# Kernel optimization log

Hardware: AMD Instinct MI355X
Metric: run time of the kernel (lower is better)

## Reference

```python
import jax, jax.numpy as jnp
import numpy as np

N_NODES = 20000
N_EDGES = 320000
F_IN = 128
H = 4        # heads per layer
D = 128      # per-head hidden dim
NEG_SLOPE = 0.2


def setup_inputs() -> dict:
    key = jax.random.key(0)
    ks = jax.random.split(key, 14)
    s = 0.05
    inp = {
        "feats": jax.random.normal(ks[0], (N_NODES, F_IN), jnp.float32),
        "src": jax.random.randint(ks[1], (N_EDGES,), 0, N_NODES, jnp.int64),
        "dst": jax.random.randint(ks[2], (N_EDGES,), 0, N_NODES, jnp.int64),
        # layer 1: in F_IN -> H heads x D, flatten agg
        "W1": s * jax.random.normal(ks[3], (F_IN, H * D), jnp.float32),
        "al1": s * jax.random.normal(ks[4], (H, D), jnp.float32),
        "ar1": s * jax.random.normal(ks[5], (H, D), jnp.float32),
        "b1": jnp.zeros((H * D,), jnp.float32),
        # layer 2: in H*D -> H heads x D, mean agg
        "W2": s * jax.random.normal(ks[6], (H * D, H * D), jnp.float32),
        "al2": s * jax.random.normal(ks[7], (H, D), jnp.float32),
        "ar2": s * jax.random.normal(ks[8], (H, D), jnp.float32),
        "b2": jnp.zeros((H * D,), jnp.float32),
        # readout Linear(D, 1)
        "Wr": s * jax.random.normal(ks[9], (D, 1), jnp.float32),
        "br": jnp.zeros((1,), jnp.float32),
    }
    return inp


def _gat_conv(x, src, dst, W, al, ar, b, n_nodes):
    """dgl GATConv: per-head linear, edge softmax over incoming edges, scatter-sum."""
    h, d = al.shape
    z = (x @ W).reshape(n_nodes, h, d)                      # [N,H,D]
    el = jnp.einsum('nhd,hd->nh', z, al)                    # [N,H]
    er = jnp.einsum('nhd,hd->nh', z, ar)                    # [N,H]
    e = jax.nn.leaky_relu(el[src] + er[dst], NEG_SLOPE)     # [E,H]
    # numerically stable softmax grouped by destination node
    emax = jax.lax.stop_gradient(jax.ops.segment_max(e, dst, num_segments=n_nodes))
    a = jnp.exp(e - emax[dst])                              # [E,H]
    denom = jax.ops.segment_sum(a, dst, num_segments=n_nodes)
    alpha = a / jnp.maximum(denom[dst], 1e-9)               # [E,H]
    out = jax.ops.segment_sum(alpha[:, :, None] * z[src], dst, num_segments=n_nodes)
    return out + b.reshape(1, h, d)                         # [N,H,D]


def reference(feats, src, dst, W1, al1, ar1, b1, W2, al2, ar2, b2, Wr, br):
    n = feats.shape[0]
    h1 = _gat_conv(feats, src, dst, W1, al1, ar1, b1, n)    # [N,H,D]
    h1 = jax.nn.elu(h1.reshape(n, -1))                      # flatten heads -> [N,H*D]
    h2 = _gat_conv(h1, src, dst, W2, al2, ar2, b2, n)       # [N,H,D]
    h2 = h2.mean(axis=1)                                    # mean over heads -> [N,D]
    node_preds = h2 @ Wr + br                               # [N,1]
    return node_preds.sum(axis=0)                           # [1]
```

## Files before the change

kernel.cpp:

```cpp
#include <hip/hip_runtime.h>
#include <hip/hip_bf16.h>
#include <cstddef>

constexpr int NN = 20000;
constexpr int NE = 320000;
constexpr int NHEAD = 4;
constexpr int ND = 128;
constexpr int HD = 512;
constexpr int MPAD = 20096;
constexpr int SLOTS = 64;
constexpr float NEG_SLOPE = 0.2f;

using short8 = __attribute__((ext_vector_type(8))) short;
using f32x4 = __attribute__((ext_vector_type(4))) float;
using f32x2 = __attribute__((ext_vector_type(2))) float;

__device__ inline void gload16(const void* g, void* l) {
  __builtin_amdgcn_global_load_lds(
      (const __attribute__((address_space(1))) void*)g,
      (__attribute__((address_space(3))) void*)l, 16, 0, 0);
}

__device__ inline unsigned char f32_to_fp8(float v) {
  int pk = __builtin_amdgcn_cvt_pk_fp8_f32(v, v, 0, false);
  return (unsigned char)(pk & 0xff);
}

constexpr int S0 = NE;
constexpr int S1 = S0 + MPAD * 128;
constexpr int S2 = S1 + 512 * 128;
constexpr int S3 = S2 + 12 * 512;
constexpr int S4 = S3 + 256;
__global__ __launch_bounds__(256) void prep_kernel(
    const float* __restrict__ feats, const float* __restrict__ W1,
    const float* __restrict__ W2, const float* __restrict__ al2,
    const float* __restrict__ ar2, const float* __restrict__ Wr,
    const int* __restrict__ src, const int* __restrict__ dst,
    __hip_bfloat16* __restrict__ featsb, __hip_bfloat16* __restrict__ W1t,
    float* __restrict__ vcomb, float* __restrict__ partials,
    int* __restrict__ cnt, int* __restrict__ src_perm) {
  int t = blockIdx.x * 256 + threadIdx.x;
  if (t < S0) {
    int d = dst[t];
    int p = atomicAdd(&cnt[d], 1);
    if (p < SLOTS) src_perm[d * SLOTS + p] = src[t];
  } else if (t < S1) {
    int u = t - S0;
    featsb[u] = __float2bfloat16(u < NN * 128 ? feats[u] : 0.f);
  } else if (t < S2) {
    int u = t - S1;
    W1t[u] = __float2bfloat16(W1[(size_t)(u & 127) * 512 + (u >> 7)]);
  } else if (t < S3) {
    int u = t - S2;
    int v = u >> 9, k = u & 511;
    int h = (v < 4) ? v : (v < 8) ? v - 4 : v - 8;
    const float* vec = (v < 4) ? (al2 + h * 128)
                     : (v < 8) ? (ar2 + h * 128) : Wr;
    const float* wrow = W2 + (size_t)k * 512 + h * 128;
    float s = 0.f;
    for (int d = 0; d < 128; ++d) s += wrow[d] * vec[d];
    vcomb[u] = s;
  } else if (t < S4) {
    partials[t - S3] = 0.f;
  }
}

__global__ __launch_bounds__(256) void gemm1_kernel(
    const __hip_bfloat16* __restrict__ A,
    const __hip_bfloat16* __restrict__ Bt,
    unsigned char* __restrict__ C,
    const float* __restrict__ al, const float* __restrict__ ar,
    float* __restrict__ el, float* __restrict__ er) {
  constexpr int K = 128;
  __shared__ short As[128 * 32];
  __shared__ short Bs[128 * 32];
  __shared__ float elbuf[4][128];
  __shared__ float erbuf[4][128];
  int t = threadIdx.x;
  int lane = t & 63;
  int wave = t >> 6;
  int rowBase = blockIdx.x * 128;
  int head = blockIdx.y;
  int colBase = head * 128;
  int woffr = (wave & 1) * 64;
  int woffc = (wave >> 1) * 64;
  int mrow = lane & 15, quad = lane >> 4;

  f32x4 acc[4][4];
#pragma unroll
  for (int i = 0; i < 4; ++i)
#pragma unroll
    for (int j = 0; j < 4; ++j) acc[i][j] = (f32x4){0.f, 0.f, 0.f, 0.f};

  for (int k0 = 0; k0 < K; k0 += 32) {
#pragma unroll
    for (int p = 0; p < 2; ++p) {
      int f = p * 256 + wave * 64 + lane;
      int r = f >> 2, kc = f & 3;
      gload16(A + (size_t)(rowBase + r) * K + k0 + kc * 8,
              As + p * 2048 + wave * 512);
      gload16(Bt + (size_t)(colBase + r) * K + k0 + kc * 8,
              Bs + p * 2048 + wave * 512);
    }
    __syncthreads();
    short8 af[4], bfr[4];
#pragma unroll
    for (int i = 0; i < 4; ++i)
      af[i] = *(const short8*)&As[(woffr + i * 16 + mrow) * 32 + quad * 8];
#pragma unroll
    for (int j = 0; j < 4; ++j)
      bfr[j] = *(const short8*)&Bs[(woffc + j * 16 + mrow) * 32 + quad * 8];
#pragma unroll
    for (int i = 0; i < 4; ++i)
#pragma unroll
      for (int j = 0; j < 4; ++j)
        acc[i][j] = __builtin_amdgcn_mfma_f32_16x16x32_bf16(af[i], bfr[j], acc[i][j], 0, 0, 0);
    __syncthreads();
  }

#pragma unroll
  for (int i = 0; i < 4; ++i) {
#pragma unroll
    for (int j = 0; j < 4; ++j) {
      int col = colBase + woffc + j * 16 + mrow;
#pragma unroll
      for (int r = 0; r < 4; ++r) {
        int row = rowBase + woffr + i * 16 + quad * 4 + r;
        C[(size_t)row * HD + col] = f32_to_fp8(acc[i][j][r]);
      }
    }
  }

  float al_v[4], ar_v[4];
#pragma unroll
  for (int j = 0; j < 4; ++j) {
    int coll = woffc + j * 16 + mrow;
    al_v[j] = al[head * 128 + coll];
    ar_v[j] = ar[head * 128 + coll];
  }
#pragma unroll
  for (int i = 0; i < 4; ++i) {
#pragma unroll
    for (int r = 0; r < 4; ++r) {
      float pl = 0.f, pr = 0.f;
#pragma unroll
      for (int j = 0; j < 4; ++j) {
        float v = acc[i][j][r];
        pl += v * al_v[j];
        pr += v * ar_v[j];
      }
#pragma unroll
      for (int off = 1; off < 16; off <<= 1) {
        pl += __shfl_xor(pl, off);
        pr += __shfl_xor(pr, off);
      }
      if (mrow == 0) {
        int row128 = woffr + i * 16 + quad * 4 + r;
        elbuf[wave][row128] = pl;
        erbuf[wave][row128] = pr;
      }
    }
  }
  __syncthreads();
  if (t < 128) {
    int row = t;
    int w0 = (row < 64) ? 0 : 1;
    float ev = elbuf[w0][row] + elbuf[w0 + 2][row];
    float rv = erbuf[w0][row] + erbuf[w0 + 2][row];
    int gr = rowBase + row;
    if (gr < NN) {
      el[gr * 4 + head] = ev;
      er[gr * 4 + head] = rv;
    }
  }
}

__global__ __launch_bounds__(256) void aggregate_kernel(
    const unsigned char* __restrict__ zf8,
    const int* __restrict__ cnt,
    const int* __restrict__ src_perm,
    const float* __restrict__ el,
    const float* __restrict__ er,
    const float* __restrict__ b1,
    const float* __restrict__ vcomb,
    float* __restrict__ el2,
    float* __restrict__ er2,
    float* __restrict__ q2) {
  __shared__ float4 alds[4][SLOTS];
  int wv = __builtin_amdgcn_readfirstlane((int)(threadIdx.x >> 6));
  int n = blockIdx.x * 4 + wv;
  int lane = threadIdx.x & 63;
  int c = min(cnt[n], SLOTS);
  int base = n * SLOTS;

  {
    float4 er4 = *reinterpret_cast<const float4*>(&er[n * 4]);
    float a0 = 0.f, a1 = 0.f, a2 = 0.f, a3 = 0.f;
    if (lane < c) {
      int s = src_perm[base + lane];
      float4 e4 = *reinterpret_cast<const float4*>(&el[s * 4]);
      float x0 = e4.x + er4.x, x1 = e4.y + er4.y;
      float x2 = e4.z + er4.z, x3 = e4.w + er4.w;
      x0 = (x0 > 0.f) ? x0 : NEG_SLOPE * x0;
      x1 = (x1 > 0.f) ? x1 : NEG_SLOPE * x1;
      x2 = (x2 > 0.f) ? x2 : NEG_SLOPE * x2;
      x3 = (x3 > 0.f) ? x3 : NEG_SLOPE * x3;
      a0 = __expf(x0); a1 = __expf(x1); a2 = __expf(x2); a3 = __expf(x3);
    }
    float s0 = a0, s1 = a1, s2 = a2, s3 = a3;
#pragma unroll
    for (int off = 1; off < 64; off <<= 1) {
      s0 += __shfl_xor(s0, off);
      s1 += __shfl_xor(s1, off);
      s2 += __shfl_xor(s2, off);
      s3 += __shfl_xor(s3, off);
    }
    float4 av;
    av.x = a0 / fmaxf(s0, 1e-9f);
    av.y = a1 / fmaxf(s1, 1e-9f);
    av.z = a2 / fmaxf(s2, 1e-9f);
    av.w = a3 / fmaxf(s3, 1e-9f);
    alds[wv][lane] = av;
  }

  int head = lane >> 4;
  float acc[8] = {};

#define EDGE_BODY(IDX)                                                         \
  {                                                                            \
    int s = src_perm[base + (IDX)];                                            \
    float4 a4 = alds[wv][(IDX)];                                               \
    float a = (head & 2) ? ((head & 1) ? a4.w : a4.z)                          \
                         : ((head & 1) ? a4.y : a4.x);                         \
    uint2 w = *reinterpret_cast<const uint2*>(zf8 + (size_t)s * 512 + lane * 8); \
    f32x2 f0 = __builtin_amdgcn_cvt_pk_f32_fp8(w.x, false);                    \
    f32x2 f1 = __builtin_amdgcn_cvt_pk_f32_fp8(w.x, true);                     \
    f32x2 f2 = __builtin_amdgcn_cvt_pk_f32_fp8(w.y, false);                    \
    f32x2 f3 = __builtin_amdgcn_cvt_pk_f32_fp8(w.y, true);                     \
    acc[0] += a * f0.x; acc[1] += a * f0.y;                                    \
    acc[2] += a * f1.x; acc[3] += a * f1.y;                                    \
    acc[4] += a * f2.x; acc[5] += a * f2.y;                                    \
    acc[6] += a * f3.x; acc[7] += a * f3.y;                                    \
  }

  int i = 0;
  for (; i + 3 < c; i += 4) {
    EDGE_BODY(i)
    EDGE_BODY(i + 1)
    EDGE_BODY(i + 2)
    EDGE_BODY(i + 3)
  }
  for (; i < c; ++i) EDGE_BODY(i)
#undef EDGE_BODY

  float4 bA = *reinterpret_cast<const float4*>(&b1[lane * 8]);
  float4 bB = *reinterpret_cast<const float4*>(&b1[lane * 8 + 4]);
  float v[8];
  v[0] = acc[0] + bA.x; v[1] = acc[1] + bA.y;
  v[2] = acc[2] + bA.z; v[3] = acc[3] + bA.w;
  v[4] = acc[4] + bB.x; v[5] = acc[5] + bB.y;
  v[6] = acc[6] + bB.z; v[7] = acc[7] + bB.w;
#pragma unroll
  for (int j = 0; j < 8; ++j) v[j] = (v[j] > 0.f) ? v[j] : expm1f(v[j]);

  float r[12];
#pragma unroll
  for (int vv = 0; vv < 12; ++vv) {
    const float* vb = vcomb + vv * 512 + lane * 8;
    float4 cA = *reinterpret_cast<const float4*>(vb);
    float4 cB = *reinterpret_cast<const float4*>(vb + 4);
    float p = v[0] * cA.x + v[1] * cA.y + v[2] * cA.z + v[3] * cA.w +
              v[4] * cB.x + v[5] * cB.y + v[6] * cB.z + v[7] * cB.w;
#pragma unroll
    for (int off = 1; off < 64; off <<= 1) p += __shfl_xor(p, off);
    r[vv] = p;
  }
  if (lane == 0) {
    *reinterpret_cast<float4*>(&el2[n * 4]) = make_float4(r[0], r[1], r[2], r[3]);
    *reinterpret_cast<float4*>(&er2[n * 4]) = make_float4(r[4], r[5], r[6], r[7]);
    *reinterpret_cast<float4*>(&q2[n * 4]) = make_float4(r[8], r[9], r[10], r[11]);
  }
}

__global__ __launch_bounds__(256) void attn_q_kernel(
    const int* __restrict__ src_perm,
    const int* __restrict__ cnt,
    const float* __restrict__ el,
    const float* __restrict__ er,
    const float* __restrict__ q,
    float* __restrict__ partials) {
  __shared__ float blk[4];
  int wv = __builtin_amdgcn_readfirstlane((int)(threadIdx.x >> 6));
  int n = blockIdx.x * 4 + wv;
  int lane = threadIdx.x & 63;
  int c = min(cnt[n], SLOTS);
  float4 er4 = *reinterpret_cast<const float4*>(&er[n * 4]);
  float a0 = 0.f, a1 = 0.f, a2 = 0.f, a3 = 0.f;
  int s = 0;
  if (lane < c) {
    s = src_perm[n * SLOTS + lane];
    float4 e4 = *reinterpret_cast<const float4*>(&el[s * 4]);
    float x0 = e4.x + er4.x, x1 = e4.y + er4.y;
    float x2 = e4.z + er4.z, x3 = e4.w + er4.w;
    x0 = (x0 > 0.f) ? x0 : NEG_SLOPE * x0;
    x1 = (x1 > 0.f) ? x1 : NEG_SLOPE * x1;
    x2 = (x2 > 0.f) ? x2 : NEG_SLOPE * x2;
    x3 = (x3 > 0.f) ? x3 : NEG_SLOPE * x3;
    a0 = __expf(x0); a1 = __expf(x1); a2 = __expf(x2); a3 = __expf(x3);
  }
  float s0 = a0, s1 = a1, s2 = a2, s3 = a3;
#pragma unroll
  for (int off = 1; off < 64; off <<= 1) {
    s0 += __shfl_xor(s0, off);
    s1 += __shfl_xor(s1, off);
    s2 += __shfl_xor(s2, off);
    s3 += __shfl_xor(s3, off);
  }
  float p = 0.f;
  if (lane < c) {
    float4 q4 = *reinterpret_cast<const float4*>(&q[s * 4]);
    p = (a0 / fmaxf(s0, 1e-9f)) * q4.x + (a1 / fmaxf(s1, 1e-9f)) * q4.y +
        (a2 / fmaxf(s2, 1e-9f)) * q4.z + (a3 / fmaxf(s3, 1e-9f)) * q4.w;
  }
#pragma unroll
  for (int off = 32; off > 0; off >>= 1) p += __shfl_down(p, off);
  if (lane == 0) blk[wv] = p;
  __syncthreads();
  if (threadIdx.x == 0) {
    atomicAdd(&partials[blockIdx.x & 255], blk[0] + blk[1] + blk[2] + blk[3]);
  }
}

__global__ __launch_bounds__(512) void final_kernel(
    const float* __restrict__ partials, const float* __restrict__ b2,
    const float* __restrict__ Wr, const float* __restrict__ br,
    float* __restrict__ out) {
  __shared__ float tmp[512];
  int t = threadIdx.x;
  float sum = (t < 256) ? partials[t] : 0.f;
  sum += (float)NN * b2[t] * Wr[t & 127];
  tmp[t] = sum;
  __syncthreads();
  for (int off = 256; off > 0; off >>= 1) {
    if (t < off) tmp[t] += tmp[t + off];
    __syncthreads();
  }
  if (t == 0) out[0] = 0.25f * tmp[0] + (float)NN * br[0];
}

extern "C" void kernel_launch(void* const* d_in, const int* in_sizes, int n_in,
                              void* d_out, int out_size, void* d_ws, size_t ws_size,
                              hipStream_t stream) {
  const float* feats = (const float*)d_in[0];
  const int* src = (const int*)d_in[1];
  const int* dst = (const int*)d_in[2];
  const float* W1 = (const float*)d_in[3];
  const float* al1 = (const float*)d_in[4];
  const float* ar1 = (const float*)d_in[5];
  const float* b1 = (const float*)d_in[6];
  const float* W2 = (const float*)d_in[7];
  const float* al2 = (const float*)d_in[8];
  const float* ar2 = (const float*)d_in[9];
  const float* b2 = (const float*)d_in[10];
  const float* Wr = (const float*)d_in[11];
  const float* br = (const float*)d_in[12];
  float* out = (float*)d_out;

  __hip_bfloat16* featsb = (__hip_bfloat16*)d_ws;
  unsigned char* zf8 = (unsigned char*)(featsb + (size_t)MPAD * 128);
  __hip_bfloat16* W1t = (__hip_bfloat16*)(zf8 + (size_t)MPAD * HD);
  float* vcomb = (float*)(W1t + 512 * 128);
  float* el1 = vcomb + 12 * 512;
  float* er1 = el1 + (size_t)NN * NHEAD;
  float* el2 = er1 + (size_t)NN * NHEAD;
  float* er2 = el2 + (size_t)NN * NHEAD;
  float* q2 = er2 + (size_t)NN * NHEAD;
  float* partials = q2 + (size_t)NN * NHEAD;
  int* cnt = (int*)(partials + 256 + 4);
  int* src_perm = cnt + NN;

  hipMemsetAsync(cnt, 0, NN * sizeof(int), stream);
  prep_kernel<<<(S4 + 255) / 256, 256, 0, stream>>>(
      feats, W1, W2, al2, ar2, Wr, src, dst, featsb, W1t, vcomb, partials,
      cnt, src_perm);

  dim3 gemm_grid(MPAD / 128, NHEAD);

  gemm1_kernel<<<gemm_grid, 256, 0, stream>>>(featsb, W1t, zf8, al1, ar1, el1, er1);

  aggregate_kernel<<<NN / 4, 256, 0, stream>>>(zf8, cnt, src_perm, el1, er1, b1,
                                               vcomb, el2, er2, q2);

  attn_q_kernel<<<NN / 4, 256, 0, stream>>>(src_perm, cnt, el2, er2, q2, partials);
  final_kernel<<<1, 512, 0, stream>>>(partials, b2, Wr, br, out);
}
```

Before: 178.8 us.

## Fuse edge bucketing into GEMM kernel, drop memset, transpose attention LDS layout

The per-destination edge bucketing (atomic slot assignment into src_perm) moves out of the prep kernel into the start of the GEMM1 kernel as a grid-stride loop. Zeroing of cnt is folded into prep, which removes the separate memset launch. In the aggregation kernel, attention weights are stored head-major in padded LDS so each lane reads its head's scalar directly instead of selecting a component from a float4, and the edge loop is unrolled by 8. This drops one launch and shrinks prep. The cost is extra atomic traffic inside the GEMM kernel and more registers in the aggregation loop.

```diff
diff --git a/kernel.cpp b/kernel.cpp
--- a/kernel.cpp
+++ b/kernel.cpp
@@ -26,7 +26,7 @@
   return (unsigned char)(pk & 0xff);
 }
 
-constexpr int S0 = NE;
+constexpr int S0 = NN;
 constexpr int S1 = S0 + MPAD * 128;
 constexpr int S2 = S1 + 512 * 128;
 constexpr int S3 = S2 + 12 * 512;
@@ -35,15 +35,12 @@
     const float* __restrict__ feats, const float* __restrict__ W1,
     const float* __restrict__ W2, const float* __restrict__ al2,
     const float* __restrict__ ar2, const float* __restrict__ Wr,
-    const int* __restrict__ src, const int* __restrict__ dst,
     __hip_bfloat16* __restrict__ featsb, __hip_bfloat16* __restrict__ W1t,
     float* __restrict__ vcomb, float* __restrict__ partials,
-    int* __restrict__ cnt, int* __restrict__ src_perm) {
+    int* __restrict__ cnt) {
   int t = blockIdx.x * 256 + threadIdx.x;
   if (t < S0) {
-    int d = dst[t];
-    int p = atomicAdd(&cnt[d], 1);
-    if (p < SLOTS) src_perm[d * SLOTS + p] = src[t];
+    cnt[t] = 0;
   } else if (t < S1) {
     int u = t - S0;
     featsb[u] = __float2bfloat16(u < NN * 128 ? feats[u] : 0.f);
@@ -70,13 +67,26 @@
     const __hip_bfloat16* __restrict__ Bt,
     unsigned char* __restrict__ C,
     const float* __restrict__ al, const float* __restrict__ ar,
-    float* __restrict__ el, float* __restrict__ er) {
+    float* __restrict__ el, float* __restrict__ er,
+    const int* __restrict__ src, const int* __restrict__ dst,
+    int* __restrict__ cnt, int* __restrict__ src_perm) {
   constexpr int K = 128;
   __shared__ short As[128 * 32];
   __shared__ short Bs[128 * 32];
   __shared__ float elbuf[4][128];
   __shared__ float erbuf[4][128];
   int t = threadIdx.x;
+
+  {
+    int nth = gridDim.x * gridDim.y * 256;
+    int gid = (blockIdx.y * gridDim.x + blockIdx.x) * 256 + t;
+    for (int e = gid; e < NE; e += nth) {
+      int d = dst[e];
+      int p = atomicAdd(&cnt[d], 1);
+      if (p < SLOTS) src_perm[d * SLOTS + p] = src[e];
+    }
+  }
+
   int lane = t & 63;
   int wave = t >> 6;
   int rowBase = blockIdx.x * 128;
@@ -186,7 +196,7 @@
     float* __restrict__ el2,
     float* __restrict__ er2,
     float* __restrict__ q2) {
-  __shared__ float4 alds[4][SLOTS];
+  __shared__ float aldsT[4][4][66];
   int wv = __builtin_amdgcn_readfirstlane((int)(threadIdx.x >> 6));
   int n = blockIdx.x * 4 + wv;
   int lane = threadIdx.x & 63;
@@ -215,23 +225,20 @@
       s2 += __shfl_xor(s2, off);
       s3 += __shfl_xor(s3, off);
     }
-    float4 av;
-    av.x = a0 / fmaxf(s0, 1e-9f);
-    av.y = a1 / fmaxf(s1, 1e-9f);
-    av.z = a2 / fmaxf(s2, 1e-9f);
-    av.w = a3 / fmaxf(s3, 1e-9f);
-    alds[wv][lane] = av;
+    aldsT[wv][0][lane] = a0 / fmaxf(s0, 1e-9f);
+    aldsT[wv][1][lane] = a1 / fmaxf(s1, 1e-9f);
+    aldsT[wv][2][lane] = a2 / fmaxf(s2, 1e-9f);
+    aldsT[wv][3][lane] = a3 / fmaxf(s3, 1e-9f);
   }
 
   int head = lane >> 4;
+  const float* arow = &aldsT[wv][head][0];
   float acc[8] = {};
 
 #define EDGE_BODY(IDX)                                                         \
   {                                                                            \
     int s = src_perm[base + (IDX)];                                            \
-    float4 a4 = alds[wv][(IDX)];                                               \
-    float a = (head & 2) ? ((head & 1) ? a4.w : a4.z)                          \
-                         : ((head & 1) ? a4.y : a4.x);                         \
+    float a = arow[(IDX)];                                                     \
     uint2 w = *reinterpret_cast<const uint2*>(zf8 + (size_t)s * 512 + lane * 8); \
     f32x2 f0 = __builtin_amdgcn_cvt_pk_f32_fp8(w.x, false);                    \
     f32x2 f1 = __builtin_amdgcn_cvt_pk_f32_fp8(w.x, true);                     \
@@ -244,11 +251,15 @@
   }
 
   int i = 0;
-  for (; i + 3 < c; i += 4) {
+  for (; i + 7 < c; i += 8) {
     EDGE_BODY(i)
     EDGE_BODY(i + 1)
     EDGE_BODY(i + 2)
     EDGE_BODY(i + 3)
+    EDGE_BODY(i + 4)
+    EDGE_BODY(i + 5)
+    EDGE_BODY(i + 6)
+    EDGE_BODY(i + 7)
   }
   for (; i < c; ++i) EDGE_BODY(i)
 #undef EDGE_BODY
@@ -379,14 +390,13 @@
   int* cnt = (int*)(partials + 256 + 4);
   int* src_perm = cnt + NN;
 
-  hipMemsetAsync(cnt, 0, NN * sizeof(int), stream);
   prep_kernel<<<(S4 + 255) / 256, 256, 0, stream>>>(
-      feats, W1, W2, al2, ar2, Wr, src, dst, featsb, W1t, vcomb, partials,
-      cnt, src_perm);
+      feats, W1, W2, al2, ar2, Wr, featsb, W1t, vcomb, partials, cnt);
 
   dim3 gemm_grid(MPAD / 128, NHEAD);
 
-  gemm1_kernel<<<gemm_grid, 256, 0, stream>>>(featsb, W1t, zf8, al1, ar1, el1, er1);
+  gemm1_kernel<<<gemm_grid, 256, 0, stream>>>(featsb, W1t, zf8, al1, ar1,
+                                              el1, er1, src, dst, cnt, src_perm);
 
   aggregate_kernel<<<NN / 4, 256, 0, stream>>>(zf8, cnt, src_perm, el1, er1, b1,
                                                vcomb, el2, er2, q2);
```

Measured after the change: 176.4 us. Within noise of the previous version (-1.4%).
